# Performance work log

Measured on AMD Instinct MI355X. Metric: run time of the kernel, lower is better.

## Reference

```python
import jax, jax.numpy as jnp
import numpy as np

N, IN_DIM, H1, H2, LIN, MAX_INDEX = 16384, 64, 256, 256, 64, 256


def _init_layer(key, out_dim, in_dim):
    # mimic kaiming_uniform(a=sqrt(5)) + uniform bias bound = 1/sqrt(fan_in)
    kW, kb = jax.random.split(key)
    bound_w = 1.0 / np.sqrt(in_dim)  # gain*sqrt(3/fan_in) with a=sqrt(5) -> 1/sqrt(fan_in)
    W = jax.random.uniform(kW, (MAX_INDEX, out_dim, in_dim), jnp.float32, -bound_w, bound_w)
    b = jax.random.uniform(kb, (MAX_INDEX, out_dim), jnp.float32, -bound_w, bound_w)
    return W, b


def setup_inputs() -> dict:
    key = jax.random.key(0)
    kx, ki, k1, k2, k3 = jax.random.split(key, 5)
    x = jax.random.normal(kx, (N, IN_DIM), jnp.float32)
    ind = jax.random.randint(ki, (N,), 0, MAX_INDEX, jnp.int64 if jax.config.jax_enable_x64 else jnp.int32)
    W1, b1 = _init_layer(k1, H1, IN_DIM)
    W2, b2 = _init_layer(k2, H2, H1)
    Wl, bl = _init_layer(k3, LIN, H2)
    return {"x": x, "ind": ind, "W1": W1, "b1": b1, "W2": W2, "b2": b2, "Wl": Wl, "bl": bl}


def _index_linear(x, ind, W, b):
    # per-row expert weight gather then row-wise matvec: out[n] = W[ind[n]] @ x[n] + b[ind[n]]
    return jnp.einsum('noi,ni->no', W[ind], x) + b[ind]


def reference(x, ind, W1, b1, W2, b2, Wl, bl):
    h = jnp.tanh(_index_linear(x, ind, W1, b1))
    h = jnp.tanh(_index_linear(h, ind, W2, b2))
    return _index_linear(h, ind, Wl, bl)
```

## Files before the change

kernel.cpp:

```cpp
#include <hip/hip_runtime.h>
#include <math.h>

#define NROWS   16384
#define IN_DIM  64
#define HID     256
#define OUT_DIM 64
#define NEXP    256
#define MT      64
#define HP      264

typedef __attribute__((ext_vector_type(8))) short short8;
typedef __attribute__((ext_vector_type(4))) float f32x4;
typedef __attribute__((ext_vector_type(4))) unsigned uint4v;
typedef __attribute__((ext_vector_type(2))) unsigned uint2v;


__global__ __launch_bounds__(1024) void prep_k(const int* __restrict__ ind,
                                               int* __restrict__ rows,
                                               int* __restrict__ offsets) {
  __shared__ int hist[NEXP];
  __shared__ int scan[NEXP];
  __shared__ int cur[NEXP];
  int t = threadIdx.x;
  if (t < NEXP) hist[t] = 0;
  __syncthreads();
  for (int n = t; n < NROWS; n += 1024) atomicAdd(&hist[ind[n]], 1);
  __syncthreads();
  if (t < NEXP) scan[t] = hist[t];
  __syncthreads();
  for (int d = 1; d < NEXP; d <<= 1) {
    int v = (t < NEXP && t >= d) ? scan[t - d] : 0;
    __syncthreads();
    if (t < NEXP) scan[t] += v;
    __syncthreads();
  }
  if (t < NEXP) {
    int exc = scan[t] - hist[t];
    offsets[t] = exc;
    cur[t] = exc;
    if (t == NEXP - 1) offsets[NEXP] = scan[t];
  }
  __syncthreads();
  for (int n = t; n < NROWS; n += 1024) {
    int p = atomicAdd(&cur[ind[n]], 1);
    rows[p] = n;
  }
}


__device__ __forceinline__ unsigned bf16_rn(float f) {
  unsigned u = __builtin_bit_cast(unsigned, f);
  unsigned r = 0x7fffu + ((u >> 16) & 1u);
  return (u + r) >> 16;
}

__device__ __forceinline__ unsigned pk2(float a, float b) {
  return bf16_rn(a) | (bf16_rn(b) << 16);
}

__device__ __forceinline__ short8 cvt8(f32x4 w0, f32x4 w1) {
  uint4v u;
  u.x = pk2(w0.x, w0.y);
  u.y = pk2(w0.z, w0.w);
  u.z = pk2(w1.x, w1.y);
  u.w = pk2(w1.z, w1.w);
  return __builtin_bit_cast(short8, u);
}

__device__ __forceinline__ float fast_tanh(float v) {
  float e = __expf(2.f * v);
  return 1.f - 2.f * __builtin_amdgcn_rcpf(e + 1.f);
}

template <int K, int NMT>
__device__ __forceinline__ void layer_mm(const float* __restrict__ Wp,
                                         const float* __restrict__ bp,
                                         const unsigned short* Hin,
                                         int l15, int q, f32x4 (&acc)[NMT][4]) {
#pragma unroll
  for (int mt = 0; mt < NMT; mt++) {
    f32x4 bv = *(const f32x4*)(bp + mt * 16 + q * 4);
#pragma unroll
    for (int nt = 0; nt < 4; nt++) acc[mt][nt] = bv;
  }
  const float* wr[NMT];
#pragma unroll
  for (int mt = 0; mt < NMT; mt++)
    wr[mt] = Wp + (size_t)(mt * 16 + l15) * K + q * 8;

#pragma unroll 2
  for (int ks = 0; ks < K / 32; ks++) {
    short8 bfr[4];
#pragma unroll
    for (int nt = 0; nt < 4; nt++)
      bfr[nt] = *(const short8*)&Hin[(nt * 16 + l15) * HP + ks * 32 + q * 8];
#pragma unroll
    for (int mt = 0; mt < NMT; mt++) {
      f32x4 w0 = *(const f32x4*)(wr[mt] + ks * 32);
      f32x4 w1 = *(const f32x4*)(wr[mt] + ks * 32 + 4);
      short8 a = cvt8(w0, w1);
#pragma unroll
      for (int nt = 0; nt < 4; nt++)
        acc[mt][nt] =
            __builtin_amdgcn_mfma_f32_16x16x32_bf16(a, bfr[nt], acc[mt][nt], 0, 0, 0);
    }
  }
}

__device__ __forceinline__ void write_h(f32x4 (&acc)[4][4], unsigned short* H,
                                        int w, int l15, int q) {
#pragma unroll
  for (int mt = 0; mt < 4; mt++)
#pragma unroll
    for (int nt = 0; nt < 4; nt++) {
      uint2v v;
      v.x = pk2(fast_tanh(acc[mt][nt].x), fast_tanh(acc[mt][nt].y));
      v.y = pk2(fast_tanh(acc[mt][nt].z), fast_tanh(acc[mt][nt].w));
      *(uint2v*)&H[(nt * 16 + l15) * HP + w * 64 + mt * 16 + q * 4] = v;
    }
}


__global__ __launch_bounds__(256, 2) void mlp_k(
    const float* __restrict__ x,
    const float* __restrict__ W1, const float* __restrict__ b1,
    const float* __restrict__ W2, const float* __restrict__ b2,
    const float* __restrict__ Wl, const float* __restrict__ bl,
    const int* __restrict__ rows, const int* __restrict__ offsets,
    float* __restrict__ out) {
  __shared__ __align__(16) unsigned short H[MT * HP];

  const int t = threadIdx.x;
  const int w = t >> 6;
  const int l15 = t & 15;
  const int q = (t >> 4) & 3;
  const int e = blockIdx.x >> 1;
  const int j = blockIdx.x & 1;
  const int beg = offsets[e];
  const int cnt = offsets[e + 1] - beg;

  const float* W1e = W1 + (size_t)e * HID * IN_DIM + (size_t)(w * 64) * IN_DIM;
  const float* W2e = W2 + (size_t)e * HID * HID + (size_t)(w * 64) * HID;
  const float* Wle = Wl + (size_t)e * OUT_DIM * HID + (size_t)(w * 16) * HID;
  const float* b1e = b1 + e * HID + w * 64;
  const float* b2e = b2 + e * HID + w * 64;
  const float* ble = bl + e * OUT_DIM + w * 16;

  const int sm = t >> 2;
  const int sc = (t & 3) * 16;

  for (int mt0 = j * MT; mt0 < cnt; mt0 += 2 * MT) {
    __syncthreads();
    {
      int gm = mt0 + sm;
      bool val = gm < cnt;
      int r = val ? rows[beg + gm] : 0;
      const float* xr = x + (size_t)r * IN_DIM + sc;
      uint4v u0, u1;
      if (val) {
        f32x4 a0 = *(const f32x4*)(xr);
        f32x4 a1 = *(const f32x4*)(xr + 4);
        f32x4 a2 = *(const f32x4*)(xr + 8);
        f32x4 a3 = *(const f32x4*)(xr + 12);
        u0.x = pk2(a0.x, a0.y); u0.y = pk2(a0.z, a0.w);
        u0.z = pk2(a1.x, a1.y); u0.w = pk2(a1.z, a1.w);
        u1.x = pk2(a2.x, a2.y); u1.y = pk2(a2.z, a2.w);
        u1.z = pk2(a3.x, a3.y); u1.w = pk2(a3.z, a3.w);
      } else {
        u0 = (uint4v){0, 0, 0, 0};
        u1 = (uint4v){0, 0, 0, 0};
      }
      *(uint4v*)&H[sm * HP + sc] = u0;
      *(uint4v*)&H[sm * HP + sc + 8] = u1;
    }
    __syncthreads();

    {
      f32x4 acc[4][4];
      layer_mm<IN_DIM, 4>(W1e, b1e, H, l15, q, acc);
      __syncthreads();
      write_h(acc, H, w, l15, q);
    }
    __syncthreads();

    {
      f32x4 acc[4][4];
      layer_mm<HID, 4>(W2e, b2e, H, l15, q, acc);
      __syncthreads();
      write_h(acc, H, w, l15, q);
    }
    __syncthreads();

    {
      f32x4 acc[1][4];
      layer_mm<HID, 1>(Wle, ble, H, l15, q, acc);
#pragma unroll
      for (int nt = 0; nt < 4; nt++) {
        int gm = mt0 + nt * 16 + l15;
        if (gm < cnt) {
          int r = rows[beg + gm];
          *(f32x4*)(out + (size_t)r * OUT_DIM + w * 16 + q * 4) = acc[0][nt];
        }
      }
    }
  }
}


extern "C" void kernel_launch(void* const* d_in, const int* in_sizes, int n_in,
                              void* d_out, int out_size, void* d_ws, size_t ws_size,
                              hipStream_t stream) {
  const float* x   = (const float*)d_in[0];
  const int*   ind = (const int*)d_in[1];
  const float* W1  = (const float*)d_in[2];
  const float* b1  = (const float*)d_in[3];
  const float* W2  = (const float*)d_in[4];
  const float* b2  = (const float*)d_in[5];
  const float* Wl  = (const float*)d_in[6];
  const float* bl  = (const float*)d_in[7];
  float* out = (float*)d_out;

  int* offsets = (int*)d_ws;
  int* rows    = (int*)d_ws + 260;

  prep_k<<<1, 1024, 0, stream>>>(ind, rows, offsets);
  mlp_k<<<NEXP * 2, 256, 0, stream>>>(x, W1, b1, W2, b2, Wl, bl, rows, offsets, out);
}
```

Measured before the change: 170.0 us.

## Stage expert weights via LDS double-buffering, one block per expert, split prep kernels

Replaces the single-block preprocessing kernel with a memset plus three multi-block kernels (histogram, scan, scatter) to parallelize row bucketing. The MLP kernel now uses one 512-thread block per expert with a 112-row tile, streaming weight slices into LDS with global_load_lds double-buffering so weights are loaded once per tile and shared across waves instead of each wave reading from global memory. The extra launches add overhead, the larger LDS footprint may lower occupancy, and padding rows to 112 wastes compute for experts with about 64 rows.

```diff
diff --git a/kernel.cpp b/kernel.cpp
--- a/kernel.cpp
+++ b/kernel.cpp
@@ -6,7 +6,8 @@
 #define HID     256
 #define OUT_DIM 64
 #define NEXP    256
-#define MT      64
+#define MT      112
+#define NT      7
 #define HP      264
 
 typedef __attribute__((ext_vector_type(8))) short short8;
@@ -15,36 +16,38 @@
 typedef __attribute__((ext_vector_type(2))) unsigned uint2v;
 
 
-__global__ __launch_bounds__(1024) void prep_k(const int* __restrict__ ind,
-                                               int* __restrict__ rows,
-                                               int* __restrict__ offsets) {
-  __shared__ int hist[NEXP];
-  __shared__ int scan[NEXP];
-  __shared__ int cur[NEXP];
+__global__ __launch_bounds__(256) void hist_k(const int* __restrict__ ind,
+                                              int* __restrict__ hist) {
+  int n = blockIdx.x * 256 + threadIdx.x;
+  atomicAdd(&hist[ind[n]], 1);
+}
+
+__global__ __launch_bounds__(256) void scan_k(const int* __restrict__ hist,
+                                              int* __restrict__ offsets,
+                                              int* __restrict__ cur) {
+  __shared__ int s[NEXP];
   int t = threadIdx.x;
-  if (t < NEXP) hist[t] = 0;
-  __syncthreads();
-  for (int n = t; n < NROWS; n += 1024) atomicAdd(&hist[ind[n]], 1);
-  __syncthreads();
-  if (t < NEXP) scan[t] = hist[t];
+  int h = hist[t];
+  s[t] = h;
   __syncthreads();
   for (int d = 1; d < NEXP; d <<= 1) {
-    int v = (t < NEXP && t >= d) ? scan[t - d] : 0;
-    __syncthreads();
-    if (t < NEXP) scan[t] += v;
-    __syncthreads();
-  }
-  if (t < NEXP) {
-    int exc = scan[t] - hist[t];
-    offsets[t] = exc;
-    cur[t] = exc;
-    if (t == NEXP - 1) offsets[NEXP] = scan[t];
-  }
-  __syncthreads();
-  for (int n = t; n < NROWS; n += 1024) {
-    int p = atomicAdd(&cur[ind[n]], 1);
-    rows[p] = n;
-  }
+    int v = (t >= d) ? s[t - d] : 0;
+    __syncthreads();
+    s[t] += v;
+    __syncthreads();
+  }
+  int exc = s[t] - h;
+  offsets[t] = exc;
+  cur[t] = exc;
+  if (t == NEXP - 1) offsets[NEXP] = s[t];
+}
+
+__global__ __launch_bounds__(256) void scatter_k(const int* __restrict__ ind,
+                                                 int* __restrict__ cur,
+                                                 int* __restrict__ rows) {
+  int n = blockIdx.x * 256 + threadIdx.x;
+  int p = atomicAdd(&cur[ind[n]], 1);
+  rows[p] = n;
 }
 
 
@@ -72,56 +75,74 @@
   return 1.f - 2.f * __builtin_amdgcn_rcpf(e + 1.f);
 }
 
-template <int K, int NMT>
-__device__ __forceinline__ void layer_mm(const float* __restrict__ Wp,
-                                         const float* __restrict__ bp,
-                                         const unsigned short* Hin,
-                                         int l15, int q, f32x4 (&acc)[NMT][4]) {
-#pragma unroll
-  for (int mt = 0; mt < NMT; mt++) {
-    f32x4 bv = *(const f32x4*)(bp + mt * 16 + q * 4);
-#pragma unroll
-    for (int nt = 0; nt < 4; nt++) acc[mt][nt] = bv;
-  }
-  const float* wr[NMT];
-#pragma unroll
-  for (int mt = 0; mt < NMT; mt++)
-    wr[mt] = Wp + (size_t)(mt * 16 + l15) * K + q * 8;
-
-#pragma unroll 2
-  for (int ks = 0; ks < K / 32; ks++) {
-    short8 bfr[4];
-#pragma unroll
-    for (int nt = 0; nt < 4; nt++)
-      bfr[nt] = *(const short8*)&Hin[(nt * 16 + l15) * HP + ks * 32 + q * 8];
-#pragma unroll
-    for (int mt = 0; mt < NMT; mt++) {
-      f32x4 w0 = *(const f32x4*)(wr[mt] + ks * 32);
-      f32x4 w1 = *(const f32x4*)(wr[mt] + ks * 32 + 4);
-      short8 a = cvt8(w0, w1);
-#pragma unroll
-      for (int nt = 0; nt < 4; nt++)
-        acc[mt][nt] =
-            __builtin_amdgcn_mfma_f32_16x16x32_bf16(a, bfr[nt], acc[mt][nt], 0, 0, 0);
-    }
-  }
-}
-
-__device__ __forceinline__ void write_h(f32x4 (&acc)[4][4], unsigned short* H,
-                                        int w, int l15, int q) {
-#pragma unroll
-  for (int mt = 0; mt < 4; mt++)
-#pragma unroll
-    for (int nt = 0; nt < 4; nt++) {
+template <int CPRL>
+__device__ __forceinline__ void stage_slice(const float* __restrict__ g, int krow,
+                                            int colbase, float* l, int t) {
+#pragma unroll
+  for (int r = 0; r < 4; r++) {
+    int c = r * 512 + t;
+    int row = c >> CPRL;
+    int cin = c & ((1 << CPRL) - 1);
+    const float* src = g + (size_t)row * krow + colbase + cin * 4;
+    __builtin_amdgcn_global_load_lds(
+        (const __attribute__((address_space(1))) void*)src,
+        (__attribute__((address_space(3))) void*)(l + (size_t)c * 4), 16, 0, 0);
+  }
+}
+
+__device__ __forceinline__ void slice_mm(const float* Ws, const unsigned short* Hin,
+                                         int hofs, int w, int l15, int q,
+                                         f32x4 (&acc)[2][NT]) {
+  short8 a[2];
+#pragma unroll
+  for (int mt = 0; mt < 2; mt++) {
+    const float* ap = Ws + (w * 32 + mt * 16 + l15) * 32 + q * 8;
+    a[mt] = cvt8(*(const f32x4*)ap, *(const f32x4*)(ap + 4));
+  }
+#pragma unroll
+  for (int nt = 0; nt < NT; nt++) {
+    short8 b = *(const short8*)&Hin[(nt * 16 + l15) * HP + hofs + q * 8];
+#pragma unroll
+    for (int mt = 0; mt < 2; mt++)
+      acc[mt][nt] =
+          __builtin_amdgcn_mfma_f32_16x16x32_bf16(a[mt], b, acc[mt][nt], 0, 0, 0);
+  }
+}
+
+__device__ __forceinline__ void slice_l3(const float* Ws, const unsigned short* Hin,
+                                         int ks2, int w, int l15, int q,
+                                         f32x4 (&accl)[4]) {
+#pragma unroll
+  for (int kk = 0; kk < 4; kk++) {
+    const float* ap = Ws + ((w & 3) * 16 + l15) * 128 + kk * 32 + q * 8;
+    short8 a = cvt8(*(const f32x4*)ap, *(const f32x4*)(ap + 4));
+    int hofs = ks2 * 128 + kk * 32;
+#pragma unroll
+    for (int i = 0; i < 4; i++) {
+      int nt = (w >> 2) * 4 + i;
+      if (nt < NT) {
+        short8 b = *(const short8*)&Hin[(nt * 16 + l15) * HP + hofs + q * 8];
+        accl[i] = __builtin_amdgcn_mfma_f32_16x16x32_bf16(a, b, accl[i], 0, 0, 0);
+      }
+    }
+  }
+}
+
+__device__ __forceinline__ void write_h8(f32x4 (&acc)[2][NT], unsigned short* Hd,
+                                         int w, int l15, int q) {
+#pragma unroll
+  for (int mt = 0; mt < 2; mt++)
+#pragma unroll
+    for (int nt = 0; nt < NT; nt++) {
       uint2v v;
       v.x = pk2(fast_tanh(acc[mt][nt].x), fast_tanh(acc[mt][nt].y));
       v.y = pk2(fast_tanh(acc[mt][nt].z), fast_tanh(acc[mt][nt].w));
-      *(uint2v*)&H[(nt * 16 + l15) * HP + w * 64 + mt * 16 + q * 4] = v;
-    }
-}
-
-
-__global__ __launch_bounds__(256, 2) void mlp_k(
+      *(uint2v*)&Hd[(nt * 16 + l15) * HP + w * 32 + mt * 16 + q * 4] = v;
+    }
+}
+
+
+__global__ __launch_bounds__(512, 2) void mlp_k(
     const float* __restrict__ x,
     const float* __restrict__ W1, const float* __restrict__ b1,
     const float* __restrict__ W2, const float* __restrict__ b2,
@@ -129,30 +150,35 @@
     const int* __restrict__ rows, const int* __restrict__ offsets,
     float* __restrict__ out) {
   __shared__ __align__(16) unsigned short H[MT * HP];
+  __shared__ __align__(16) float Wb[2][8192];
 
   const int t = threadIdx.x;
   const int w = t >> 6;
   const int l15 = t & 15;
   const int q = (t >> 4) & 3;
-  const int e = blockIdx.x >> 1;
-  const int j = blockIdx.x & 1;
+  const int e = blockIdx.x;
   const int beg = offsets[e];
   const int cnt = offsets[e + 1] - beg;
 
-  const float* W1e = W1 + (size_t)e * HID * IN_DIM + (size_t)(w * 64) * IN_DIM;
-  const float* W2e = W2 + (size_t)e * HID * HID + (size_t)(w * 64) * HID;
-  const float* Wle = Wl + (size_t)e * OUT_DIM * HID + (size_t)(w * 16) * HID;
-  const float* b1e = b1 + e * HID + w * 64;
-  const float* b2e = b2 + e * HID + w * 64;
-  const float* ble = bl + e * OUT_DIM + w * 16;
-
-  const int sm = t >> 2;
+  const float* W1e = W1 + (size_t)e * HID * IN_DIM;
+  const float* W2e = W2 + (size_t)e * HID * HID;
+  const float* Wle = Wl + (size_t)e * OUT_DIM * HID;
+
+  f32x4 b1v[2], b2v[2], blv;
+#pragma unroll
+  for (int mt = 0; mt < 2; mt++) {
+    b1v[mt] = *(const f32x4*)(b1 + (size_t)e * HID + w * 32 + mt * 16 + q * 4);
+    b2v[mt] = *(const f32x4*)(b2 + (size_t)e * HID + w * 32 + mt * 16 + q * 4);
+  }
+  blv = *(const f32x4*)(bl + (size_t)e * OUT_DIM + (w & 3) * 16 + q * 4);
+
+  const int sr = t >> 2;
   const int sc = (t & 3) * 16;
 
-  for (int mt0 = j * MT; mt0 < cnt; mt0 += 2 * MT) {
-    __syncthreads();
-    {
-      int gm = mt0 + sm;
+  for (int mt0 = 0; mt0 < cnt; mt0 += MT) {
+    stage_slice<3>(W1e, IN_DIM, 0, Wb[0], t);
+    if (sr < MT) {
+      int gm = mt0 + sr;
       bool val = gm < cnt;
       int r = val ? rows[beg + gm] : 0;
       const float* xr = x + (size_t)r * IN_DIM + sc;
@@ -170,39 +196,64 @@
         u0 = (uint4v){0, 0, 0, 0};
         u1 = (uint4v){0, 0, 0, 0};
       }
-      *(uint4v*)&H[sm * HP + sc] = u0;
-      *(uint4v*)&H[sm * HP + sc + 8] = u1;
-    }
-    __syncthreads();
-
-    {
-      f32x4 acc[4][4];
-      layer_mm<IN_DIM, 4>(W1e, b1e, H, l15, q, acc);
+      *(uint4v*)&H[sr * HP + sc] = u0;
+      *(uint4v*)&H[sr * HP + sc + 8] = u1;
+    }
+    __syncthreads();
+
+    f32x4 acc[2][NT];
+#pragma unroll
+    for (int mt = 0; mt < 2; mt++)
+#pragma unroll
+      for (int nt = 0; nt < NT; nt++) acc[mt][nt] = b1v[mt];
+
+    stage_slice<3>(W1e, IN_DIM, 32, Wb[1], t);
+    slice_mm(Wb[0], H, 0, w, l15, q, acc);
+    __syncthreads();
+
+    stage_slice<3>(W2e, HID, 0, Wb[0], t);
+    slice_mm(Wb[1], H, 32, w, l15, q, acc);
+    __syncthreads();
+
+    write_h8(acc, H, w, l15, q);
+    __syncthreads();
+
+#pragma unroll
+    for (int mt = 0; mt < 2; mt++)
+#pragma unroll
+      for (int nt = 0; nt < NT; nt++) acc[mt][nt] = b2v[mt];
+
+    for (int ks = 0; ks < 8; ks++) {
+      if (ks < 7) stage_slice<3>(W2e, HID, (ks + 1) * 32, Wb[(ks + 1) & 1], t);
+      else        stage_slice<5>(Wle, HID, 0, Wb[0], t);
+      slice_mm(Wb[ks & 1], H, ks * 32, w, l15, q, acc);
       __syncthreads();
-      write_h(acc, H, w, l15, q);
-    }
-    __syncthreads();
-
-    {
-      f32x4 acc[4][4];
-      layer_mm<HID, 4>(W2e, b2e, H, l15, q, acc);
-      __syncthreads();
-      write_h(acc, H, w, l15, q);
-    }
-    __syncthreads();
-
-    {
-      f32x4 acc[1][4];
-      layer_mm<HID, 1>(Wle, ble, H, l15, q, acc);
-#pragma unroll
-      for (int nt = 0; nt < 4; nt++) {
+    }
+
+    write_h8(acc, H, w, l15, q);
+    __syncthreads();
+
+    f32x4 accl[4];
+#pragma unroll
+    for (int i = 0; i < 4; i++) accl[i] = blv;
+
+    stage_slice<5>(Wle, HID, 128, Wb[1], t);
+    slice_l3(Wb[0], H, 0, w, l15, q, accl);
+    __syncthreads();
+    slice_l3(Wb[1], H, 1, w, l15, q, accl);
+
+#pragma unroll
+    for (int i = 0; i < 4; i++) {
+      int nt = (w >> 2) * 4 + i;
+      if (nt < NT) {
         int gm = mt0 + nt * 16 + l15;
         if (gm < cnt) {
           int r = rows[beg + gm];
-          *(f32x4*)(out + (size_t)r * OUT_DIM + w * 16 + q * 4) = acc[0][nt];
+          *(f32x4*)(out + (size_t)r * OUT_DIM + (w & 3) * 16 + q * 4) = accl[i];
         }
       }
     }
+    __syncthreads();
   }
 }
 
@@ -221,8 +272,13 @@
   float* out = (float*)d_out;
 
   int* offsets = (int*)d_ws;
-  int* rows    = (int*)d_ws + 260;
-
-  prep_k<<<1, 1024, 0, stream>>>(ind, rows, offsets);
-  mlp_k<<<NEXP * 2, 256, 0, stream>>>(x, W1, b1, W2, b2, Wl, bl, rows, offsets, out);
-}
+  int* cur     = (int*)d_ws + 260;
+  int* hist    = (int*)d_ws + 260;
+  int* rows    = (int*)d_ws + 516;
+
+  hipMemsetAsync(hist, 0, NEXP * sizeof(int), stream);
+  hist_k<<<NROWS / 256, 256, 0, stream>>>(ind, hist);
+  scan_k<<<1, 256, 0, stream>>>(hist, offsets, cur);
+  scatter_k<<<NROWS / 256, 256, 0, stream>>>(ind, cur, rows);
+  mlp_k<<<NEXP, 512, 0, stream>>>(x, W1, b1, W2, b2, Wl, bl, rows, offsets, out);
+}
```

Result: faster. 164.7 us (-3.1%).
